# Kernel optimization log

Measured on AMD Instinct MI355X. Metric: run time of the kernel, lower is better.

The kernel has to match this reference:

```python
import jax, jax.numpy as jnp
import numpy as np

BATCH = 2048
H0, W0 = 64, 64
EMBED = 2
BOND = 16


def _layer_specs():
    """Replicates BinaryTTN.__init__ layer construction.
    Returns list of (h, w, bond, in_dim, orientation) per layer."""
    specs = []
    H, W = H0, W0
    in_dim = EMBED
    n_layers = int(round(np.log2(H0 * W0)))  # 12
    for li in range(n_layers):
        bond = 1 if li == n_layers - 1 else BOND
        orientation = H < W  # horizontal if width larger
        h = H // (1 if orientation else 2)
        w = W // (2 if orientation else 1)
        specs.append((h, w, bond, in_dim, orientation))
        H, W = h, w
        in_dim = bond
    return specs


def setup_inputs() -> dict:
    key = jax.random.key(0)
    specs = _layer_specs()
    keys = jax.random.split(key, len(specs) + 1)
    x = jax.random.normal(keys[0], (BATCH, EMBED, H0, W0), dtype=jnp.float32)
    out = {"x": x}
    for i, (h, w, bond, in_dim, _) in enumerate(specs):
        # scale 1/in_dim keeps activation variance ~1 across layers
        out[f"w{i}"] = jax.random.normal(keys[i + 1], (h, w, bond, in_dim, in_dim), dtype=jnp.float32) / in_dim
    return out


def _ttn_layer(x, W):
    # x: [n, H, W, in_dim]; W: [h, w, bond, in_dim, in_dim]
    n, Hc, Wc, d = x.shape
    h, w = W.shape[0], W.shape[1]
    if Hc == h:  # horizontal merge: pair adjacent columns
        xr = x.reshape(n, h, w, 2, d)
        left, right = xr[:, :, :, 0, :], xr[:, :, :, 1, :]
    else:  # vertical merge: pair adjacent rows
        xr = x.reshape(n, h, 2, w, d)
        left, right = xr[:, :, 0, :, :], xr[:, :, 1, :, :]
    # per-location bilinear contraction
    return jnp.einsum('xybij,nxyi,nxyj->nxyb', W, left, right)


def reference(x, w0, w1, w2, w3, w4, w5, w6, w7, w8, w9, w10, w11):
    ws = (w0, w1, w2, w3, w4, w5, w6, w7, w8, w9, w10, w11)
    h = jnp.transpose(x, (0, 2, 3, 1))  # NCHW -> NHWC
    for W in ws:
        h = _ttn_layer(h, W)
    return h  # [n, 1, 1, 1]
```

## Files before the change

### kernel.cpp

```cpp
#include <hip/hip_runtime.h>


#define NB 2048

typedef float f4 __attribute__((ext_vector_type(4)));
typedef float f32x4 __attribute__((ext_vector_type(4)));
typedef unsigned u32x4 __attribute__((ext_vector_type(4)));
typedef short bf16x8 __attribute__((ext_vector_type(8)));

#define MFMA(a, b, c) __builtin_amdgcn_mfma_f32_16x16x32_bf16(a, b, c, 0, 0, 0)

__device__ __forceinline__ unsigned pk2(float a, float b) {
  unsigned r;
  asm("v_cvt_pk_bf16_f32 %0, %1, %2" : "=v"(r) : "v"(a), "v"(b));
  return r;
}

__device__ __forceinline__ void split3(float a, float b,
                                       unsigned& h, unsigned& m, unsigned& l) {
  h = pk2(a, b);
  float ha = __uint_as_float(h << 16), hb = __uint_as_float(h & 0xffff0000u);
  float ra = a - ha, rb = b - hb;
  m = pk2(ra, rb);
  float ma = __uint_as_float(m << 16), mb = __uint_as_float(m & 0xffff0000u);
  l = pk2(ra - ma, rb - mb);
}

__device__ __forceinline__ bf16x8 asfrag(u32x4 x) {
  union { u32x4 u; bf16x8 f; } c; c.u = x; return c.f;
}

__device__ __forceinline__ void stage_w(const float* __restrict__ wsite,
                                        unsigned* FA, unsigned* A3, int tid) {
  const int sb = tid >> 4, si = tid & 15;
  const float* wp = wsite + sb * 256 + si * 16;
  f4 v0 = *(const f4*)(wp + 0), v1 = *(const f4*)(wp + 4);
  f4 v2 = *(const f4*)(wp + 8), v3 = *(const f4*)(wp + 12);
  unsigned h[8], m[8], l[8];
  split3(v0.x, v0.y, h[0], m[0], l[0]); split3(v0.z, v0.w, h[1], m[1], l[1]);
  split3(v1.x, v1.y, h[2], m[2], l[2]); split3(v1.z, v1.w, h[3], m[3], l[3]);
  split3(v2.x, v2.y, h[4], m[4], l[4]); split3(v2.z, v2.w, h[5], m[5], l[5]);
  split3(v3.x, v3.y, h[6], m[6], l[6]); split3(v3.z, v3.w, h[7], m[7], l[7]);
  unsigned* fa = FA + si * 260 + sb * 4;
  *(u32x4*)(fa + 0)   = u32x4{h[0], h[1], h[2], h[3]};
  *(u32x4*)(fa + 64)  = u32x4{h[4], h[5], h[6], h[7]};
  *(u32x4*)(fa + 128) = u32x4{m[0], m[1], m[2], m[3]};
  *(u32x4*)(fa + 192) = u32x4{m[4], m[5], m[6], m[7]};
  unsigned* a3 = A3 + si * 132 + sb * 4;
  *(u32x4*)(a3 + 0)  = u32x4{l[0], l[1], l[2], l[3]};
  *(u32x4*)(a3 + 64) = u32x4{l[4], l[5], l[6], l[7]};
}

__device__ __forceinline__ void build_b(const float r[8], int lo,
                                        u32x4& b1, u32x4& b2, u32x4& b3) {
  unsigned bh[4], bm[4], bl[4];
  split3(r[0], r[1], bh[0], bm[0], bl[0]);
  split3(r[2], r[3], bh[1], bm[1], bl[1]);
  split3(r[4], r[5], bh[2], bm[2], bl[2]);
  split3(r[6], r[7], bh[3], bm[3], bl[3]);
  u32x4 vh{bh[0], bh[1], bh[2], bh[3]};
  u32x4 vm{bm[0], bm[1], bm[2], bm[3]};
  u32x4 vl{bl[0], bl[1], bl[2], bl[3]};
  b1 = lo ? vh : vm;
  b2 = lo ? vm : vh;
  b3 = lo ? vl : vh;
}

__global__ __launch_bounds__(256) void ttn_tx(
    const float* __restrict__ x, float* __restrict__ xT)
{
  __shared__ float S[4][32][65];
  const int x1 = blockIdx.x;
  const int n0 = blockIdx.y * 32;
  const int tid = threadIdx.x;
  const int lane = tid & 63;
  const int g = tid >> 6;
  const int c = g >> 1, rrow = g & 1;

  const float* xp = x + (long)n0 * 8192 + c * 4096 + (2 * x1 + rrow) * 64 + lane;
  for (int nn = 0; nn < 32; ++nn)
    S[g][nn][lane] = xp[(long)nn * 8192];
  __syncthreads();

  const int nl = tid & 31;
  const int yg = tid >> 5;
  for (int yy = 0; yy < 4; ++yy) {
    const int y1 = yg * 4 + yy;
    float* op = xT + (long)(x1 * 32 + y1) * 8 * NB + n0 + nl;
#pragma unroll
    for (int q = 0; q < 8; ++q) {
      const int cc = q >> 2, rr2 = (q >> 1) & 1, colq = q & 1;
      op[(long)q * NB] = S[cc * 2 + rr2][nl][2 * y1 + colq];
    }
  }
}

__global__ __launch_bounds__(256, 5) void ttn_l0l1_mf(
    const float* __restrict__ xT, float* __restrict__ out,
    const float* __restrict__ w0, const float* __restrict__ w1)
{
  __shared__ unsigned FA[4160], A3[2112];
  const int s1 = blockIdx.x;
  const int x1 = s1 >> 5, y1 = s1 & 31;
  const int tid = threadIdx.x;
  stage_w(w1 + (long)s1 * 4096, FA, A3, tid);
  __syncthreads();

  const int lane = tid & 63;
  const int col = lane & 15, kg = lane >> 4, jg = kg & 1;
  const int lo = (kg < 2);
  const unsigned* fap = FA + (kg * 16 + col) * 4;
  const unsigned* fbp0 = lo ? fap : (A3 + ((kg - 2) * 16 + col) * 4);
  const int fbstr = lo ? 260 : 132;

  const float* w0s = w0 + (long)(x1 * 64 + 2 * y1) * 64;

  float wb[8][4];
#pragma unroll
  for (int jj = 0; jj < 8; ++jj) {
    f4 v = *(const f4*)(w0s + 64 + (jg * 8 + jj) * 4);
    wb[jj][0] = v.x; wb[jj][1] = v.y; wb[jj][2] = v.z; wb[jj][3] = v.w;
  }

  const float* xb = xT + (long)s1 * 8 * NB;
  const long nb0 = (long)blockIdx.y * 512 + (tid >> 6) * 32 + col;

  for (int p = 0; p < 4; ++p) {
    const long nbase = nb0 + p * 128;
    float qv[2][8];
#pragma unroll
    for (int t = 0; t < 2; ++t) {
      const float* qp = xb + nbase + t * 16;
#pragma unroll
      for (int d = 0; d < 8; ++d) qv[t][d] = qp[(long)d * NB];
    }
    u32x4 B1[2], B2[2], B3[2];
    float pa[2][4];
#pragma unroll
    for (int t = 0; t < 2; ++t) {
      const float q0 = qv[t][0], q1 = qv[t][1], q2 = qv[t][2], q3 = qv[t][3];
      const float q4 = qv[t][4], q5 = qv[t][5], q6 = qv[t][6], q7 = qv[t][7];
      pa[t][0] = q0 * q2; pa[t][1] = q0 * q6; pa[t][2] = q4 * q2; pa[t][3] = q4 * q6;
      const float pb0 = q1 * q3, pb1 = q1 * q7, pb2 = q5 * q3, pb3 = q5 * q7;
      float r[8];
#pragma unroll
      for (int jj = 0; jj < 8; ++jj)
        r[jj] = wb[jj][0] * pb0 + wb[jj][1] * pb1 +
                wb[jj][2] * pb2 + wb[jj][3] * pb3;
      build_b(r, lo, B1[t], B2[t], B3[t]);
    }
    f32x4 acc0{0.f, 0.f, 0.f, 0.f}, acc1{0.f, 0.f, 0.f, 0.f};
    const unsigned* a1 = fap;
    const unsigned* a3v = fbp0;
#pragma unroll 2
    for (int i = 0; i < 16; ++i) {
      bf16x8 af1 = asfrag(*(const u32x4*)a1);  a1 += 260;
      bf16x8 af3 = asfrag(*(const u32x4*)a3v); a3v += fbstr;
      const float u0 = w0s[i * 4 + 0], u1 = w0s[i * 4 + 1];
      const float u2 = w0s[i * 4 + 2], u3 = w0s[i * 4 + 3];
      f32x4 z{0.f, 0.f, 0.f, 0.f};
      f32x4 c0 = MFMA(af1, asfrag(B1[0]), z);
      f32x4 c1 = MFMA(af1, asfrag(B1[1]), z);
      c0 = MFMA(af1, asfrag(B2[0]), c0);
      c1 = MFMA(af1, asfrag(B2[1]), c1);
      c0 = MFMA(af3, asfrag(B3[0]), c0);
      c1 = MFMA(af3, asfrag(B3[1]), c1);
      const float lv0 = u0 * pa[0][0] + u1 * pa[0][1] + u2 * pa[0][2] + u3 * pa[0][3];
      const float lv1 = u0 * pa[1][0] + u1 * pa[1][1] + u2 * pa[1][2] + u3 * pa[1][3];
      acc0 += c0 * lv0;
      acc1 += c1 * lv1;
    }
    float* ob = out + ((long)s1 * 16 + kg * 4) * NB + nbase;
#pragma unroll
    for (int rg = 0; rg < 4; ++rg) {
      ob[(long)rg * NB] = acc0[rg];
      ob[(long)rg * NB + 16] = acc1[rg];
    }
  }
}

__global__ __launch_bounds__(256, 5) void ttn_mf(
    const float* __restrict__ in, float* __restrict__ out,
    const float* __restrict__ w, int outW, int prevW, int pairW, int np)
{
  __shared__ unsigned FA[4160], A3[2112];
  const int site = blockIdx.x;
  const int xs = site / outW, ys = site - xs * outW;
  int ls, rs;
  if (pairW) { ls = xs * prevW + 2 * ys; rs = ls + 1; }
  else       { ls = 2 * xs * prevW + ys; rs = ls + prevW; }

  const int tid = threadIdx.x;
  stage_w(w + (long)site * 4096, FA, A3, tid);
  __syncthreads();

  const int lane = tid & 63;
  const int col = lane & 15, kg = lane >> 4, jg = kg & 1;
  const int lo = (kg < 2);
  const unsigned* fap = FA + (kg * 16 + col) * 4;
  const unsigned* fbp0 = lo ? fap : (A3 + ((kg - 2) * 16 + col) * 4);
  const int fbstr = lo ? 260 : 132;

  const float* lb = in + (long)ls * 16 * NB;
  const float* rbj = in + (long)rs * 16 * NB + (long)jg * 8 * NB;

  for (int p = 0; p < np; ++p) {
    const long nbase = (long)blockIdx.y * (128 * np) + p * 128 + (tid >> 6) * 32 + col;
    u32x4 B1[2], B2[2], B3[2];
    f32x4 acc[2];
#pragma unroll
    for (int t = 0; t < 2; ++t) {
      const float* rp = rbj + nbase + t * 16;
      float r[8];
#pragma unroll
      for (int jj = 0; jj < 8; ++jj) r[jj] = rp[(long)jj * NB];
      build_b(r, lo, B1[t], B2[t], B3[t]);
      acc[t] = f32x4{0.f, 0.f, 0.f, 0.f};
    }
    const unsigned* a1 = fap;
    const unsigned* a3v = fbp0;
    const float* lp = lb + nbase;
#pragma unroll 2
    for (int i = 0; i < 16; ++i) {
      bf16x8 af1 = asfrag(*(const u32x4*)a1);  a1 += 260;
      bf16x8 af3 = asfrag(*(const u32x4*)a3v); a3v += fbstr;
      float lv0 = lp[0], lv1 = lp[16];
      lp += NB;
      f32x4 z{0.f, 0.f, 0.f, 0.f};
      f32x4 c0 = MFMA(af1, asfrag(B1[0]), z);
      f32x4 c1 = MFMA(af1, asfrag(B1[1]), z);
      c0 = MFMA(af1, asfrag(B2[0]), c0);
      c1 = MFMA(af1, asfrag(B2[1]), c1);
      c0 = MFMA(af3, asfrag(B3[0]), c0);
      c1 = MFMA(af3, asfrag(B3[1]), c1);
      acc[0] += c0 * lv0;
      acc[1] += c1 * lv1;
    }
    float* ob = out + ((long)site * 16 + kg * 4) * NB + nbase;
#pragma unroll
    for (int t = 0; t < 2; ++t)
#pragma unroll
      for (int rg = 0; rg < 4; ++rg)
        ob[(long)rg * NB + t * 16] = acc[t][rg];
  }
}

__global__ __launch_bounds__(256) void ttn_l11(
    const float* __restrict__ in, float* __restrict__ out,
    const float* __restrict__ w)
{
  __shared__ float Wl[256];
  const int tid = threadIdx.x;
  if (tid < 64)
    *(f4*)&Wl[tid * 4] = *(const f4*)(w + tid * 4);
  __syncthreads();

  const long n = (long)blockIdx.x * 256 + tid;
  float l[16], r[16];
#pragma unroll
  for (int i = 0; i < 16; ++i) l[i] = in[(long)i * NB + n];
#pragma unroll
  for (int j = 0; j < 16; ++j) r[j] = in[(long)(16 + j) * NB + n];
  float acc = 0.f;
#pragma unroll
  for (int i = 0; i < 16; ++i)
#pragma unroll
    for (int j = 0; j < 16; ++j) acc += Wl[i * 16 + j] * (l[i] * r[j]);
  out[n] = acc;
}

extern "C" void kernel_launch(void* const* d_in, const int* in_sizes, int n_in,
                              void* d_out, int out_size, void* d_ws, size_t ws_size,
                              hipStream_t stream) {
  const float* x = (const float*)d_in[0];
  const float* w[12];
  for (int k = 0; k < 12; ++k) w[k] = (const float*)d_in[1 + k];

  float* R0 = (float*)d_ws;
  float* R1 = R0 + (size_t)1024 * 8 * NB;

  ttn_tx<<<dim3(32, NB / 32), 256, 0, stream>>>(x, R0);
  ttn_l0l1_mf<<<dim3(1024, 4), 256, 0, stream>>>(R0, R1, w[0], w[1]);

  ttn_mf<<<dim3(512, 4), 256, 0, stream>>>(R1, R0, w[2], 32, 32, 0, 4);
  ttn_mf<<<dim3(256, 4), 256, 0, stream>>>(R0, R1, w[3], 16, 32, 1, 4);
  ttn_mf<<<dim3(128, 4), 256, 0, stream>>>(R1, R0, w[4], 16, 16, 0, 4);
  ttn_mf<<<dim3(64, 4), 256, 0, stream>>>(R0, R1, w[5], 8, 16, 1, 4);
  ttn_mf<<<dim3(32, 16), 256, 0, stream>>>(R1, R0, w[6], 8, 8, 0, 1);
  ttn_mf<<<dim3(16, 16), 256, 0, stream>>>(R0, R1, w[7], 4, 8, 1, 1);
  ttn_mf<<<dim3(8, 16), 256, 0, stream>>>(R1, R0, w[8], 4, 4, 0, 1);
  ttn_mf<<<dim3(4, 16), 256, 0, stream>>>(R0, R1, w[9], 2, 4, 1, 1);
  ttn_mf<<<dim3(2, 16), 256, 0, stream>>>(R1, R0, w[10], 2, 2, 0, 1);
  ttn_l11<<<dim3(NB / 256), 256, 0, stream>>>(R0, (float*)d_out, w[11]);
}
```

Before: 302.5 us.

## Tile activation layout into 16-sample blocks with contiguous channels

Changes the intermediate activation layout from channel-major with stride NB to a blocked layout where each tile of 16 samples keeps all channels contiguous (16x16 floats per site-tile). The transpose, fused L0/L1, generic MFMA, and final layer kernels are all updated to read and write this layout consistently. The goal is better locality: each wave's loads and stores for one sample tile fall in a 1 KB contiguous block instead of strided rows far apart, cutting TLB and DRAM page spread. The trade-off is 64B-per-row accesses spread across channels, so coalescing per instruction stays similar.

```diff
diff --git a/kernel.cpp b/kernel.cpp
--- a/kernel.cpp
+++ b/kernel.cpp
@@ -84,13 +84,15 @@
 
   const int nl = tid & 31;
   const int yg = tid >> 5;
+  const int n = n0 + nl;
+  const long toff = (long)(n >> 4) * 128 + (n & 15);
   for (int yy = 0; yy < 4; ++yy) {
     const int y1 = yg * 4 + yy;
-    float* op = xT + (long)(x1 * 32 + y1) * 8 * NB + n0 + nl;
+    float* op = xT + (long)(x1 * 32 + y1) * 8 * NB + toff;
 #pragma unroll
     for (int q = 0; q < 8; ++q) {
       const int cc = q >> 2, rr2 = (q >> 1) & 1, colq = q & 1;
-      op[(long)q * NB] = S[cc * 2 + rr2][nl][2 * y1 + colq];
+      op[q * 16] = S[cc * 2 + rr2][nl][2 * y1 + colq];
     }
   }
 }
@@ -123,16 +125,17 @@
   }
 
   const float* xb = xT + (long)s1 * 8 * NB;
-  const long nb0 = (long)blockIdx.y * 512 + (tid >> 6) * 32 + col;
+  float* outb = out + (long)s1 * 16 * NB;
+  const int nt0 = blockIdx.y * 32 + (tid >> 6) * 2;
 
   for (int p = 0; p < 4; ++p) {
-    const long nbase = nb0 + p * 128;
+    const int ntp = nt0 + p * 8;
     float qv[2][8];
 #pragma unroll
     for (int t = 0; t < 2; ++t) {
-      const float* qp = xb + nbase + t * 16;
-#pragma unroll
-      for (int d = 0; d < 8; ++d) qv[t][d] = qp[(long)d * NB];
+      const float* qp = xb + (long)(ntp + t) * 128 + col;
+#pragma unroll
+      for (int d = 0; d < 8; ++d) qv[t][d] = qp[d * 16];
     }
     u32x4 B1[2], B2[2], B3[2];
     float pa[2][4];
@@ -170,11 +173,12 @@
       acc0 += c0 * lv0;
       acc1 += c1 * lv1;
     }
-    float* ob = out + ((long)s1 * 16 + kg * 4) * NB + nbase;
+    float* ob0 = outb + (long)(ntp + 0) * 256 + kg * 64 + col;
+    float* ob1 = outb + (long)(ntp + 1) * 256 + kg * 64 + col;
 #pragma unroll
     for (int rg = 0; rg < 4; ++rg) {
-      ob[(long)rg * NB] = acc0[rg];
-      ob[(long)rg * NB + 16] = acc1[rg];
+      ob0[rg * 16] = acc0[rg];
+      ob1[rg * 16] = acc1[rg];
     }
   }
 }
@@ -202,30 +206,31 @@
   const int fbstr = lo ? 260 : 132;
 
   const float* lb = in + (long)ls * 16 * NB;
-  const float* rbj = in + (long)rs * 16 * NB + (long)jg * 8 * NB;
+  const float* rb = in + (long)rs * 16 * NB;
+  float* outb = out + (long)site * 16 * NB;
+  const int nt0 = blockIdx.y * (8 * np) + (tid >> 6) * 2;
 
   for (int p = 0; p < np; ++p) {
-    const long nbase = (long)blockIdx.y * (128 * np) + p * 128 + (tid >> 6) * 32 + col;
+    const int ntp = nt0 + p * 8;
     u32x4 B1[2], B2[2], B3[2];
-    f32x4 acc[2];
 #pragma unroll
     for (int t = 0; t < 2; ++t) {
-      const float* rp = rbj + nbase + t * 16;
+      const float* rp = rb + (long)(ntp + t) * 256 + jg * 128 + col;
       float r[8];
 #pragma unroll
-      for (int jj = 0; jj < 8; ++jj) r[jj] = rp[(long)jj * NB];
+      for (int jj = 0; jj < 8; ++jj) r[jj] = rp[jj * 16];
       build_b(r, lo, B1[t], B2[t], B3[t]);
-      acc[t] = f32x4{0.f, 0.f, 0.f, 0.f};
-    }
+    }
+    f32x4 acc0{0.f, 0.f, 0.f, 0.f}, acc1{0.f, 0.f, 0.f, 0.f};
     const unsigned* a1 = fap;
     const unsigned* a3v = fbp0;
-    const float* lp = lb + nbase;
+    const float* lp0 = lb + (long)(ntp + 0) * 256 + col;
+    const float* lp1 = lb + (long)(ntp + 1) * 256 + col;
 #pragma unroll 2
     for (int i = 0; i < 16; ++i) {
       bf16x8 af1 = asfrag(*(const u32x4*)a1);  a1 += 260;
       bf16x8 af3 = asfrag(*(const u32x4*)a3v); a3v += fbstr;
-      float lv0 = lp[0], lv1 = lp[16];
-      lp += NB;
+      const float lv0 = lp0[i * 16], lv1 = lp1[i * 16];
       f32x4 z{0.f, 0.f, 0.f, 0.f};
       f32x4 c0 = MFMA(af1, asfrag(B1[0]), z);
       f32x4 c1 = MFMA(af1, asfrag(B1[1]), z);
@@ -233,15 +238,16 @@
       c1 = MFMA(af1, asfrag(B2[1]), c1);
       c0 = MFMA(af3, asfrag(B3[0]), c0);
       c1 = MFMA(af3, asfrag(B3[1]), c1);
-      acc[0] += c0 * lv0;
-      acc[1] += c1 * lv1;
-    }
-    float* ob = out + ((long)site * 16 + kg * 4) * NB + nbase;
-#pragma unroll
-    for (int t = 0; t < 2; ++t)
-#pragma unroll
-      for (int rg = 0; rg < 4; ++rg)
-        ob[(long)rg * NB + t * 16] = acc[t][rg];
+      acc0 += c0 * lv0;
+      acc1 += c1 * lv1;
+    }
+    float* ob0 = outb + (long)(ntp + 0) * 256 + kg * 64 + col;
+    float* ob1 = outb + (long)(ntp + 1) * 256 + kg * 64 + col;
+#pragma unroll
+    for (int rg = 0; rg < 4; ++rg) {
+      ob0[rg * 16] = acc0[rg];
+      ob1[rg * 16] = acc1[rg];
+    }
   }
 }
 
@@ -256,11 +262,14 @@
   __syncthreads();
 
   const long n = (long)blockIdx.x * 256 + tid;
+  const long toff = (n >> 4) * 256 + (n & 15);
+  const float* lp = in + toff;
+  const float* rp = in + (long)16 * NB + toff;
   float l[16], r[16];
 #pragma unroll
-  for (int i = 0; i < 16; ++i) l[i] = in[(long)i * NB + n];
-#pragma unroll
-  for (int j = 0; j < 16; ++j) r[j] = in[(long)(16 + j) * NB + n];
+  for (int i = 0; i < 16; ++i) l[i] = lp[i * 16];
+#pragma unroll
+  for (int j = 0; j < 16; ++j) r[j] = rp[j * 16];
   float acc = 0.f;
 #pragma unroll
   for (int i = 0; i < 16; ++i)
```

Measured after the change: 307.4 us. About the same (+1.6%).

## Switch intermediate activations to batch-major site layout with vectorized loads and stores

Applied to the files above, without the earlier changes.

Intermediate tensors change from [site][channel][batch] to [site][batch][channel], so each thread reads and writes its channel vector with 16-byte vector accesses instead of strided scalar ones. The transpose kernel drops its LDS staging and writes 8-float packed vectors directly, and every consumer kernel is updated to match. The trade-off is that neighbouring lanes now touch addresses 64 bytes apart rather than contiguous ones, which may lower coalescing efficiency per request.

```diff
diff --git a/kernel.cpp b/kernel.cpp
--- a/kernel.cpp
+++ b/kernel.cpp
@@ -69,29 +69,20 @@
 __global__ __launch_bounds__(256) void ttn_tx(
     const float* __restrict__ x, float* __restrict__ xT)
 {
-  __shared__ float S[4][32][65];
   const int x1 = blockIdx.x;
-  const int n0 = blockIdx.y * 32;
-  const int tid = threadIdx.x;
-  const int lane = tid & 63;
-  const int g = tid >> 6;
-  const int c = g >> 1, rrow = g & 1;
-
-  const float* xp = x + (long)n0 * 8192 + c * 4096 + (2 * x1 + rrow) * 64 + lane;
-  for (int nn = 0; nn < 32; ++nn)
-    S[g][nn][lane] = xp[(long)nn * 8192];
-  __syncthreads();
-
-  const int nl = tid & 31;
-  const int yg = tid >> 5;
-  for (int yy = 0; yy < 4; ++yy) {
-    const int y1 = yg * 4 + yy;
-    float* op = xT + (long)(x1 * 32 + y1) * 8 * NB + n0 + nl;
-#pragma unroll
-    for (int q = 0; q < 8; ++q) {
-      const int cc = q >> 2, rr2 = (q >> 1) & 1, colq = q & 1;
-      op[(long)q * NB] = S[cc * 2 + rr2][nl][2 * y1 + colq];
-    }
+  const int y1 = threadIdx.x & 31;
+  const int np = threadIdx.x >> 5;
+  const int n  = blockIdx.y * 16 + np * 2;
+
+  const float* xb = x + (long)n * 8192 + (2 * x1) * 64 + 2 * y1;
+#pragma unroll
+  for (int d = 0; d < 2; ++d) {
+    const float* xd = xb + d * 8192;
+    f4 q0 = {xd[0],    xd[1],    xd[64],   xd[65]};
+    f4 q1 = {xd[4096], xd[4097], xd[4160], xd[4161]};
+    float* op = xT + ((long)(x1 * 32 + y1) * NB + n + d) * 8;
+    *reinterpret_cast<f4*>(op)     = q0;
+    *reinterpret_cast<f4*>(op + 4) = q1;
   }
 }
 
@@ -122,24 +113,21 @@
     wb[jj][0] = v.x; wb[jj][1] = v.y; wb[jj][2] = v.z; wb[jj][3] = v.w;
   }
 
-  const float* xb = xT + (long)s1 * 8 * NB;
+  const float* xb8 = xT + (long)s1 * 8 * NB;
+  float* outb = out + (long)s1 * 16 * NB;
   const long nb0 = (long)blockIdx.y * 512 + (tid >> 6) * 32 + col;
 
   for (int p = 0; p < 4; ++p) {
     const long nbase = nb0 + p * 128;
-    float qv[2][8];
-#pragma unroll
-    for (int t = 0; t < 2; ++t) {
-      const float* qp = xb + nbase + t * 16;
-#pragma unroll
-      for (int d = 0; d < 8; ++d) qv[t][d] = qp[(long)d * NB];
-    }
     u32x4 B1[2], B2[2], B3[2];
     float pa[2][4];
 #pragma unroll
     for (int t = 0; t < 2; ++t) {
-      const float q0 = qv[t][0], q1 = qv[t][1], q2 = qv[t][2], q3 = qv[t][3];
-      const float q4 = qv[t][4], q5 = qv[t][5], q6 = qv[t][6], q7 = qv[t][7];
+      const float* qp = xb8 + (nbase + t * 16) * 8;
+      f4 va = *(const f4*)(qp);
+      f4 vb = *(const f4*)(qp + 4);
+      const float q0 = va.x, q1 = va.y, q2 = va.z, q3 = va.w;
+      const float q4 = vb.x, q5 = vb.y, q6 = vb.z, q7 = vb.w;
       pa[t][0] = q0 * q2; pa[t][1] = q0 * q6; pa[t][2] = q4 * q2; pa[t][3] = q4 * q6;
       const float pb0 = q1 * q3, pb1 = q1 * q7, pb2 = q5 * q3, pb3 = q5 * q7;
       float r[8];
@@ -170,12 +158,8 @@
       acc0 += c0 * lv0;
       acc1 += c1 * lv1;
     }
-    float* ob = out + ((long)s1 * 16 + kg * 4) * NB + nbase;
-#pragma unroll
-    for (int rg = 0; rg < 4; ++rg) {
-      ob[(long)rg * NB] = acc0[rg];
-      ob[(long)rg * NB + 16] = acc1[rg];
-    }
+    *(f4*)(outb + (nbase + 0)  * 16 + kg * 4) = acc0;
+    *(f4*)(outb + (nbase + 16) * 16 + kg * 4) = acc1;
   }
 }
 
@@ -202,46 +186,46 @@
   const int fbstr = lo ? 260 : 132;
 
   const float* lb = in + (long)ls * 16 * NB;
-  const float* rbj = in + (long)rs * 16 * NB + (long)jg * 8 * NB;
+  const float* rb = in + (long)rs * 16 * NB;
+  float* outb = out + (long)site * 16 * NB;
+  const long nb0 = (long)blockIdx.y * (128 * np) + (tid >> 6) * 32 + col;
 
   for (int p = 0; p < np; ++p) {
-    const long nbase = (long)blockIdx.y * (128 * np) + p * 128 + (tid >> 6) * 32 + col;
+    const long nbase = nb0 + p * 128;
     u32x4 B1[2], B2[2], B3[2];
-    f32x4 acc[2];
 #pragma unroll
     for (int t = 0; t < 2; ++t) {
-      const float* rp = rbj + nbase + t * 16;
-      float r[8];
-#pragma unroll
-      for (int jj = 0; jj < 8; ++jj) r[jj] = rp[(long)jj * NB];
+      const float* rp = rb + (nbase + t * 16) * 16 + jg * 8;
+      f4 ra = *(const f4*)(rp);
+      f4 rc = *(const f4*)(rp + 4);
+      float r[8] = {ra.x, ra.y, ra.z, ra.w, rc.x, rc.y, rc.z, rc.w};
       build_b(r, lo, B1[t], B2[t], B3[t]);
-      acc[t] = f32x4{0.f, 0.f, 0.f, 0.f};
-    }
+    }
+    f32x4 acc0{0.f, 0.f, 0.f, 0.f}, acc1{0.f, 0.f, 0.f, 0.f};
     const unsigned* a1 = fap;
     const unsigned* a3v = fbp0;
-    const float* lp = lb + nbase;
-#pragma unroll 2
-    for (int i = 0; i < 16; ++i) {
-      bf16x8 af1 = asfrag(*(const u32x4*)a1);  a1 += 260;
-      bf16x8 af3 = asfrag(*(const u32x4*)a3v); a3v += fbstr;
-      float lv0 = lp[0], lv1 = lp[16];
-      lp += NB;
-      f32x4 z{0.f, 0.f, 0.f, 0.f};
-      f32x4 c0 = MFMA(af1, asfrag(B1[0]), z);
-      f32x4 c1 = MFMA(af1, asfrag(B1[1]), z);
-      c0 = MFMA(af1, asfrag(B2[0]), c0);
-      c1 = MFMA(af1, asfrag(B2[1]), c1);
-      c0 = MFMA(af3, asfrag(B3[0]), c0);
-      c1 = MFMA(af3, asfrag(B3[1]), c1);
-      acc[0] += c0 * lv0;
-      acc[1] += c1 * lv1;
-    }
-    float* ob = out + ((long)site * 16 + kg * 4) * NB + nbase;
-#pragma unroll
-    for (int t = 0; t < 2; ++t)
-#pragma unroll
-      for (int rg = 0; rg < 4; ++rg)
-        ob[(long)rg * NB + t * 16] = acc[t][rg];
+    const float* lp0 = lb + (nbase + 0)  * 16;
+    const float* lp1 = lb + (nbase + 16) * 16;
+    for (int ic = 0; ic < 4; ++ic) {
+      const f4 lv0 = *(const f4*)(lp0 + ic * 4);
+      const f4 lv1 = *(const f4*)(lp1 + ic * 4);
+#pragma unroll
+      for (int ii = 0; ii < 4; ++ii) {
+        bf16x8 af1 = asfrag(*(const u32x4*)a1);  a1 += 260;
+        bf16x8 af3 = asfrag(*(const u32x4*)a3v); a3v += fbstr;
+        f32x4 z{0.f, 0.f, 0.f, 0.f};
+        f32x4 c0 = MFMA(af1, asfrag(B1[0]), z);
+        f32x4 c1 = MFMA(af1, asfrag(B1[1]), z);
+        c0 = MFMA(af1, asfrag(B2[0]), c0);
+        c1 = MFMA(af1, asfrag(B2[1]), c1);
+        c0 = MFMA(af3, asfrag(B3[0]), c0);
+        c1 = MFMA(af3, asfrag(B3[1]), c1);
+        acc0 += c0 * lv0[ii];
+        acc1 += c1 * lv1[ii];
+      }
+    }
+    *(f4*)(outb + (nbase + 0)  * 16 + kg * 4) = acc0;
+    *(f4*)(outb + (nbase + 16) * 16 + kg * 4) = acc1;
   }
 }
 
@@ -256,11 +240,16 @@
   __syncthreads();
 
   const long n = (long)blockIdx.x * 256 + tid;
+  const float* lp = in + n * 16;
+  const float* rp = in + (long)16 * NB + n * 16;
   float l[16], r[16];
 #pragma unroll
-  for (int i = 0; i < 16; ++i) l[i] = in[(long)i * NB + n];
-#pragma unroll
-  for (int j = 0; j < 16; ++j) r[j] = in[(long)(16 + j) * NB + n];
+  for (int c = 0; c < 4; ++c) {
+    f4 lv = *(const f4*)(lp + 4 * c);
+    f4 rv = *(const f4*)(rp + 4 * c);
+    l[4 * c + 0] = lv.x; l[4 * c + 1] = lv.y; l[4 * c + 2] = lv.z; l[4 * c + 3] = lv.w;
+    r[4 * c + 0] = rv.x; r[4 * c + 1] = rv.y; r[4 * c + 2] = rv.z; r[4 * c + 3] = rv.w;
+  }
   float acc = 0.f;
 #pragma unroll
   for (int i = 0; i < 16; ++i)
@@ -279,7 +268,7 @@
   float* R0 = (float*)d_ws;
   float* R1 = R0 + (size_t)1024 * 8 * NB;
 
-  ttn_tx<<<dim3(32, NB / 32), 256, 0, stream>>>(x, R0);
+  ttn_tx<<<dim3(32, NB / 16), 256, 0, stream>>>(x, R0);
   ttn_l0l1_mf<<<dim3(1024, 4), 256, 0, stream>>>(R0, R1, w[0], w[1]);
 
   ttn_mf<<<dim3(512, 4), 256, 0, stream>>>(R1, R0, w[2], 32, 32, 0, 4);
```

Result: slower. 325.9 us (+7.7%).
